# Optimization experiments

Measured on AMD Instinct MI355X. Metric: run time of the kernel, lower is better.

Reference implementation:

```python
import jax, jax.numpy as jnp
import numpy as np

N = 50000
E = 800000
IN_D, HID_D, EMB_D, K = 128, 128, 64, 16
ALPHA = 1.0
NEG_SLOPE = 0.2


def _l2norm(x, eps=1e-12):
    n = jnp.sqrt(jnp.sum(x * x, axis=1, keepdims=True))
    return x / jnp.maximum(n, eps)


def _gat(x, src, dst, W, a_src, a_dst, b, n_nodes):
    # PyG GATConv, heads=1: h = xW; e_ij = leakyrelu(a_src.h_j + a_dst.h_i)
    h = x @ W                                   # [N, D]
    al_s = h @ a_src                            # [N]
    al_d = h @ a_dst                            # [N]
    logits = jax.nn.leaky_relu(al_s[src] + al_d[dst], NEG_SLOPE)  # [E']
    m = jax.ops.segment_max(logits, dst, num_segments=n_nodes)
    ex = jnp.exp(logits - m[dst])
    denom = jax.ops.segment_sum(ex, dst, num_segments=n_nodes)
    alpha = ex / denom[dst]                     # softmax over incoming edges
    out = jax.ops.segment_sum(h[src] * alpha[:, None], dst, num_segments=n_nodes)
    return out + b


def _cluster_prob(z, cluster):
    z2 = jnp.sum(z * z, axis=1, keepdims=True)          # [N,1]
    c2 = jnp.sum(cluster * cluster, axis=1)[None, :]    # [1,K]
    dist = z2 + c2 - 2.0 * (z @ cluster.T)              # [N,K]
    q = 1.0 / (1.0 + dist / ALPHA)
    q = (q + 1e-07) ** ((ALPHA + 1.0) / 2.0)
    return q / jnp.sum(q, axis=1, keepdims=True)


def setup_inputs() -> dict:
    key = jax.random.key(0)
    ks = jax.random.split(key, 20)
    d = {}
    d['x'] = jax.random.normal(ks[0], (N, IN_D), dtype=jnp.float32)
    d['edge_index'] = jax.random.randint(ks[1], (2, E), 0, N, dtype=jnp.int32)
    dims = [(IN_D, HID_D), (HID_D, EMB_D), (EMB_D, HID_D), (HID_D, IN_D)]
    for i, (di, do) in enumerate(dims):
        s = 1.0 / np.sqrt(di)
        d[f'W{i+1}'] = jax.random.normal(ks[2 + 4 * i], (di, do), dtype=jnp.float32) * s
        d[f'a{i+1}s'] = jax.random.normal(ks[3 + 4 * i], (do,), dtype=jnp.float32) * 0.1
        d[f'a{i+1}d'] = jax.random.normal(ks[4 + 4 * i], (do,), dtype=jnp.float32) * 0.1
        d[f'b{i+1}'] = jnp.zeros((do,), dtype=jnp.float32)
    d['cluster'] = jax.random.normal(ks[18], (K, EMB_D), dtype=jnp.float32) * 0.1
    return d


def reference(x, edge_index, W1, a1s, a1d, b1, W2, a2s, a2d, b2,
              W3, a3s, a3d, b3, W4, a4s, a4d, b4, cluster):
    # add self loops (PyG GATConv default)
    loop = jnp.arange(N, dtype=edge_index.dtype)
    src = jnp.concatenate([edge_index[0], loop])
    dst = jnp.concatenate([edge_index[1], loop])

    xn = _l2norm(x)
    h1 = jax.nn.relu(_gat(xn, src, dst, W1, a1s, a1d, b1, N))
    z = _gat(h1, src, dst, W2, a2s, a2d, b2, N)
    z = _l2norm(z)
    d1 = jax.nn.relu(_gat(z, src, dst, W3, a3s, a3d, b3, N))
    x_hat = _gat(d1, src, dst, W4, a4s, a4d, b4, N)
    q = _cluster_prob(z, cluster)
    return (z, x_hat, q)
```

## Files before the change

kernel.cpp:

```cpp
#include <hip/hip_runtime.h>

#define NN 50000
#define NE 800000
#define NBK 196
#define BCAP 8192
#define GEMM_GRID 391
#define WTOT 49152

typedef unsigned int uint;
typedef unsigned short ushort;
typedef __attribute__((ext_vector_type(8))) short short8v;
typedef __attribute__((ext_vector_type(4))) float float4v;

static __device__ __forceinline__ float waveReduceSum(float v) {
#pragma unroll
  for (int o = 32; o > 0; o >>= 1) v += __shfl_xor(v, o);
  return v;
}
static __device__ __forceinline__ float waveReduceMax(float v) {
#pragma unroll
  for (int o = 32; o > 0; o >>= 1) v = fmaxf(v, __shfl_xor(v, o));
  return v;
}
static __device__ __forceinline__ float bf_lo(uint u) { return __uint_as_float(u << 16); }
static __device__ __forceinline__ float bf_hi(uint u) { return __uint_as_float(u & 0xffff0000u); }
static __device__ __forceinline__ uint f2bf(float f) {
  uint u = __float_as_uint(f);
  return (u + 0x7fffu + ((u >> 16) & 1u)) >> 16;
}
static __device__ __forceinline__ int waveInclScan(int v, int lane) {
#pragma unroll
  for (int o = 1; o < 64; o <<= 1) {
    int u = __shfl_up(v, o);
    if (lane >= o) v += u;
  }
  return v;
}
static __device__ __forceinline__ void split8(const float* f, short8v& hi, short8v& lo) {
#pragma unroll
  for (int j = 0; j < 8; ++j) {
    uint h = f2bf(f[j]);
    hi[j] = (short)h;
    float hf = __uint_as_float(h << 16);
    lo[j] = (short)f2bf(f[j] - hf);
  }
}

__global__ void k_zero(int* bcnt) {
  if (threadIdx.x < NBK) bcnt[threadIdx.x] = 0;
}
__global__ __launch_bounds__(256) void k_bucket(
    const int* __restrict__ esrc, const int* __restrict__ edst,
    uint* __restrict__ ebuf, int* __restrict__ bcnt) {
  __shared__ int hist[NBK];
  __shared__ int gbase[NBK];
  int tid = threadIdx.x;
  for (int i = tid; i < NBK; i += 256) hist[i] = 0;
  __syncthreads();
  const int ET = NE + NN;
  int base = blockIdx.x * 4096;
  int myb[16];
  uint mypk[16];
#pragma unroll
  for (int j = 0; j < 16; ++j) {
    int e = base + j * 256 + tid;
    int s, d;
    if (e < NE) { s = esrc[e]; d = edst[e]; }
    else if (e < ET) { s = e - NE; d = s; }
    else { myb[j] = -1; continue; }
    int b = d >> 8;
    myb[j] = b;
    mypk[j] = (uint)s | ((uint)(d & 255) << 16);
    atomicAdd(&hist[b], 1);
  }
  __syncthreads();
  for (int i = tid; i < NBK; i += 256) {
    int h = hist[i];
    gbase[i] = h > 0 ? atomicAdd(&bcnt[i], h) : 0;
    hist[i] = 0;
  }
  __syncthreads();
#pragma unroll
  for (int j = 0; j < 16; ++j) {
    int b = myb[j];
    if (b < 0) continue;
    int r = atomicAdd(&hist[b], 1);
    int pos = gbase[b] + r;
    if (pos < BCAP) ebuf[(size_t)b * BCAP + pos] = mypk[j];
  }
}
__global__ __launch_bounds__(256) void k_csr(
    const uint* __restrict__ ebuf, const int* __restrict__ bcnt,
    int* __restrict__ indptr, int* __restrict__ srcs) {
  __shared__ int h[256];
  __shared__ int cur[256];
  __shared__ int wsm[4];
  __shared__ int bbs;
  int tid = threadIdx.x, b = blockIdx.x;
  int lane = tid & 63, wv = tid >> 6;
  int v = (tid < NBK) ? bcnt[tid] : 0;
  int inc = waveInclScan(v, lane);
  if (lane == 63) wsm[wv] = inc;
  __syncthreads();
  int woff = 0;
  for (int k = 0; k < wv; ++k) woff += wsm[k];
  if (tid == b) bbs = inc - v + woff;
  h[tid] = 0;
  __syncthreads();
  int bbase = bbs;
  int cnt = bcnt[b];
  const uint* eb = ebuf + (size_t)b * BCAP;
  for (int i = tid; i < cnt; i += 256) atomicAdd(&h[eb[i] >> 16], 1);
  __syncthreads();
  int hv = h[tid];
  int inc2 = waveInclScan(hv, lane);
  if (lane == 63) wsm[wv] = inc2;
  __syncthreads();
  int woff2 = 0;
  for (int k = 0; k < wv; ++k) woff2 += wsm[k];
  int nodeExcl = inc2 - hv + woff2;
  int node = b * 256 + tid;
  if (node < NN) indptr[node] = bbase + nodeExcl;
  if (node == NN - 1) indptr[NN] = bbase + nodeExcl + hv;
  cur[tid] = nodeExcl;
  __syncthreads();
  for (int i = tid; i < cnt; i += 256) {
    uint pk = eb[i];
    int r = atomicAdd(&cur[pk >> 16], 1);
    srcs[bbase + r] = (int)(pk & 0xffffu);
  }
}

__global__ void k_wprep(const float* __restrict__ W1, const float* __restrict__ W2,
                        const float* __restrict__ W3, const float* __restrict__ W4,
                        ushort* __restrict__ hi, ushort* __restrict__ lo) {
  int i = blockIdx.x * 256 + threadIdx.x;
  if (i >= WTOT) return;
  const float* W; int DO, base;
  if (i < 16384)      { W = W1; DO = 128; base = 0; }
  else if (i < 24576) { W = W2; DO = 64;  base = 16384; }
  else if (i < 32768) { W = W3; DO = 128; base = 24576; }
  else                { W = W4; DO = 128; base = 32768; }
  int idx = i - base;
  int k = idx / DO, col = idx % DO;
  float w = W[idx];
  uint h = f2bf(w);
  float hf = __uint_as_float(h << 16);
  uint l2 = f2bf(w - hf);
  int CT = DO >> 4;
  int fo = base + (((k >> 5) * CT + (col >> 4)) * 64 + ((col & 15) | (((k >> 3) & 3) << 4))) * 8 + (k & 7);
  hi[fo] = (ushort)h;
  lo[fo] = (ushort)l2;
}

template <int K, int DO, bool NORM>
__global__ __launch_bounds__(256) void k_gemm_mfma(
    const float* __restrict__ X, const ushort* __restrict__ Whi,
    const ushort* __restrict__ Wlo,
    const float* __restrict__ avs, const float* __restrict__ avd,
    ushort* __restrict__ H, float* __restrict__ als, float* __restrict__ ald, int n) {
  constexpr int KS = K / 32, CT = DO / 16;
  constexpr int W4N = K * DO / 8;
  __shared__ ushort sWhi[K * DO];
  __shared__ ushort sWlo[K * DO];
  __shared__ float sas[DO], sad[DO];
  int tid = threadIdx.x;
  for (int i = tid; i < DO; i += 256) { sas[i] = avs[i]; sad[i] = avd[i]; }
  {
    const uint4* ghi = (const uint4*)Whi;
    const uint4* glo = (const uint4*)Wlo;
    uint4* shi = (uint4*)sWhi;
    uint4* slo = (uint4*)sWlo;
    for (int i = tid; i < W4N; i += 256) { shi[i] = ghi[i]; slo[i] = glo[i]; }
  }
  __syncthreads();
  int lane = tid & 63, wv = tid >> 6;
  int ntiles = (n + 63) >> 6;
  for (int tile = blockIdx.x; tile < ntiles; tile += gridDim.x) {
    int r0 = tile * 64 + wv * 16;
    if (r0 >= n) continue;
    int row = r0 + (lane & 15);
    int sub = lane >> 4;
    const float* xrow = X + (size_t)row * K;
    float xr[KS][8];
#pragma unroll
    for (int s = 0; s < KS; ++s) {
      *(float4*)&xr[s][0] = *(const float4*)(xrow + s * 32 + sub * 8);
      *(float4*)&xr[s][4] = *(const float4*)(xrow + s * 32 + sub * 8 + 4);
    }
    if (NORM) {
      float ss = 0.f;
#pragma unroll
      for (int s = 0; s < KS; ++s)
#pragma unroll
        for (int j = 0; j < 8; ++j) ss += xr[s][j] * xr[s][j];
      ss += __shfl_xor(ss, 16);
      ss += __shfl_xor(ss, 32);
      float sc = 1.0f / fmaxf(sqrtf(ss), 1e-12f);
#pragma unroll
      for (int s = 0; s < KS; ++s)
#pragma unroll
        for (int j = 0; j < 8; ++j) xr[s][j] *= sc;
    }
    float4v acc[CT];
#pragma unroll
    for (int c = 0; c < CT; ++c) acc[c] = (float4v){0.f, 0.f, 0.f, 0.f};
#pragma unroll
    for (int s = 0; s < KS; ++s) {
      short8v ahi, alo;
      split8(xr[s], ahi, alo);
#pragma unroll
      for (int c = 0; c < CT; ++c) {
        short8v bhi = *(const short8v*)&sWhi[(s * CT + c) * 512 + lane * 8];
        short8v blo = *(const short8v*)&sWlo[(s * CT + c) * 512 + lane * 8];
        acc[c] = __builtin_amdgcn_mfma_f32_16x16x32_bf16(ahi, bhi, acc[c], 0, 0, 0);
        acc[c] = __builtin_amdgcn_mfma_f32_16x16x32_bf16(ahi, blo, acc[c], 0, 0, 0);
        acc[c] = __builtin_amdgcn_mfma_f32_16x16x32_bf16(alo, bhi, acc[c], 0, 0, 0);
      }
    }
    int rbase = r0 + (sub << 2);
    float alsp[4] = {0.f, 0.f, 0.f, 0.f};
    float aldp[4] = {0.f, 0.f, 0.f, 0.f};
#pragma unroll
    for (int c = 0; c < CT; ++c) {
      int col = (c << 4) + (lane & 15);
      float as_ = sas[col], ad_ = sad[col];
#pragma unroll
      for (int j = 0; j < 4; ++j) {
        float v = acc[c][j];
        alsp[j] += v * as_;
        aldp[j] += v * ad_;
        uint bv = f2bf(v);
        uint nb = __shfl_xor(bv, 1);
        if (!(lane & 1)) {
          *(uint*)&H[(size_t)(rbase + j) * DO + col] = bv | (nb << 16);
        }
      }
    }
#pragma unroll
    for (int j = 0; j < 4; ++j) {
      float vs = alsp[j], vd = aldp[j];
#pragma unroll
      for (int o = 1; o < 16; o <<= 1) { vs += __shfl_xor(vs, o); vd += __shfl_xor(vd, o); }
      if ((lane & 15) == 0) { als[rbase + j] = vs; ald[rbase + j] = vd; }
    }
  }
}

template <int D, int MODE>
__global__ __launch_bounds__(256) void k_attn_aggr(
    const int* __restrict__ indptr, const int* __restrict__ srcs,
    const float* __restrict__ als, const float* __restrict__ ald,
    const ushort* __restrict__ H, const float* __restrict__ bias,
    float* __restrict__ out, const float* __restrict__ cluster,
    float* __restrict__ qout, int n) {
  constexpr int CAP = 256;
  __shared__ float slg[4][CAP];
  __shared__ int ssrc[4][CAP];
  __shared__ float scl[MODE == 2 ? 1024 : 4];
  __shared__ float sz[4][MODE == 2 ? 64 : 4];
  int w = (blockIdx.x * blockDim.x + threadIdx.x) >> 6;
  int l = threadIdx.x & 63;
  int wv = threadIdx.x >> 6;
  if (MODE == 2) {
    for (int i = threadIdx.x; i < 1024; i += 256) scl[i] = cluster[i];
    __syncthreads();
  }
  if (w >= n) return;
  int s0 = indptr[w], s1 = indptr[w + 1];
  int deg = s1 - s0;
  float ad = ald[w];
  float inv;
  float ax = 0.f, ay = 0.f, az = 0.f, aw = 0.f;
  const uint2* Hr = (const uint2*)H;
  if (deg <= CAP) {
    float mx = -1e30f;
    for (int t = l; t < deg; t += 64) {
      int s = srcs[s0 + t];
      float v = als[s] + ad;
      v = v >= 0.f ? v : 0.2f * v;
      ssrc[wv][t] = s;
      slg[wv][t] = v;
      mx = fmaxf(mx, v);
    }
    mx = waveReduceMax(mx);
    float sum = 0.f;
    for (int t = l; t < deg; t += 64) {
      float e = __expf(slg[wv][t] - mx);
      slg[wv][t] = e;
      sum += e;
    }
    sum = waveReduceSum(sum);
    inv = 1.0f / sum;
    if (D == 128) {
      int g = l >> 5, j = l & 31;
      int i = 0;
      for (; i + 16 <= deg; i += 16) {
        float p[8]; int e[8]; uint2 u[8];
#pragma unroll
        for (int r = 0; r < 8; ++r) { int idx = i + 2 * r + g; p[r] = slg[wv][idx]; e[r] = ssrc[wv][idx]; }
#pragma unroll
        for (int r = 0; r < 8; ++r) u[r] = Hr[(size_t)e[r] * 32 + j];
#pragma unroll
        for (int r = 0; r < 8; ++r) {
          ax += p[r] * bf_lo(u[r].x); ay += p[r] * bf_hi(u[r].x);
          az += p[r] * bf_lo(u[r].y); aw += p[r] * bf_hi(u[r].y);
        }
      }
      for (; i + 8 <= deg; i += 8) {
        float p[4]; int e[4]; uint2 u[4];
#pragma unroll
        for (int r = 0; r < 4; ++r) { int idx = i + 2 * r + g; p[r] = slg[wv][idx]; e[r] = ssrc[wv][idx]; }
#pragma unroll
        for (int r = 0; r < 4; ++r) u[r] = Hr[(size_t)e[r] * 32 + j];
#pragma unroll
        for (int r = 0; r < 4; ++r) {
          ax += p[r] * bf_lo(u[r].x); ay += p[r] * bf_hi(u[r].x);
          az += p[r] * bf_lo(u[r].y); aw += p[r] * bf_hi(u[r].y);
        }
      }
      for (; i < deg; i += 2) {
        int idx = i + g;
        if (idx < deg) {
          float p = slg[wv][idx];
          uint2 u = Hr[(size_t)ssrc[wv][idx] * 32 + j];
          ax += p * bf_lo(u.x); ay += p * bf_hi(u.x);
          az += p * bf_lo(u.y); aw += p * bf_hi(u.y);
        }
      }
    } else {
      int g = l >> 4, j = l & 15;
      int i = 0;
      for (; i + 32 <= deg; i += 32) {
        float p[8]; int e[8]; uint2 u[8];
#pragma unroll
        for (int r = 0; r < 8; ++r) { int idx = i + 4 * r + g; p[r] = slg[wv][idx]; e[r] = ssrc[wv][idx]; }
#pragma unroll
        for (int r = 0; r < 8; ++r) u[r] = Hr[(size_t)e[r] * 16 + j];
#pragma unroll
        for (int r = 0; r < 8; ++r) {
          ax += p[r] * bf_lo(u[r].x); ay += p[r] * bf_hi(u[r].x);
          az += p[r] * bf_lo(u[r].y); aw += p[r] * bf_hi(u[r].y);
        }
      }
      for (; i + 16 <= deg; i += 16) {
        float p[4]; int e[4]; uint2 u[4];
#pragma unroll
        for (int r = 0; r < 4; ++r) { int idx = i + 4 * r + g; p[r] = slg[wv][idx]; e[r] = ssrc[wv][idx]; }
#pragma unroll
        for (int r = 0; r < 4; ++r) u[r] = Hr[(size_t)e[r] * 16 + j];
#pragma unroll
        for (int r = 0; r < 4; ++r) {
          ax += p[r] * bf_lo(u[r].x); ay += p[r] * bf_hi(u[r].x);
          az += p[r] * bf_lo(u[r].y); aw += p[r] * bf_hi(u[r].y);
        }
      }
      for (; i < deg; i += 4) {
        int idx = i + g;
        if (idx < deg) {
          float p = slg[wv][idx];
          uint2 u = Hr[(size_t)ssrc[wv][idx] * 16 + j];
          ax += p * bf_lo(u.x); ay += p * bf_hi(u.x);
          az += p * bf_lo(u.y); aw += p * bf_hi(u.y);
        }
      }
    }
  } else {
    float mx = -1e30f;
    for (int t = l; t < deg; t += 64) {
      int s = srcs[s0 + t];
      float v = als[s] + ad;
      v = v >= 0.f ? v : 0.2f * v;
      mx = fmaxf(mx, v);
    }
    mx = waveReduceMax(mx);
    float sum = 0.f;
    for (int t = l; t < deg; t += 64) {
      int s = srcs[s0 + t];
      float v = als[s] + ad;
      v = v >= 0.f ? v : 0.2f * v;
      sum += __expf(v - mx);
    }
    sum = waveReduceSum(sum);
    inv = 1.0f / sum;
    for (int base = 0; base < deg; base += 64) {
      int t = base + l;
      if (t < deg) {
        int s = srcs[s0 + t];
        float v = als[s] + ad;
        v = v >= 0.f ? v : 0.2f * v;
        ssrc[wv][l] = s;
        slg[wv][l] = __expf(v - mx);
      }
      __builtin_amdgcn_wave_barrier();
      int m = min(64, deg - base);
      if (D == 128) {
        int g = l >> 5, j = l & 31;
        for (int i2 = g; i2 < m; i2 += 2) {
          float p = slg[wv][i2];
          uint2 u = Hr[(size_t)ssrc[wv][i2] * 32 + j];
          ax += p * bf_lo(u.x); ay += p * bf_hi(u.x);
          az += p * bf_lo(u.y); aw += p * bf_hi(u.y);
        }
      } else {
        int g = l >> 4, j = l & 15;
        for (int i2 = g; i2 < m; i2 += 4) {
          float p = slg[wv][i2];
          uint2 u = Hr[(size_t)ssrc[wv][i2] * 16 + j];
          ax += p * bf_lo(u.x); ay += p * bf_hi(u.x);
          az += p * bf_lo(u.y); aw += p * bf_hi(u.y);
        }
      }
      __builtin_amdgcn_wave_barrier();
    }
  }
  if (D == 128) {
    ax += __shfl_xor(ax, 32); ay += __shfl_xor(ay, 32);
    az += __shfl_xor(az, 32); aw += __shfl_xor(aw, 32);
    if (l < 32) {
      float4 bv = ((const float4*)bias)[l];
      float v0 = ax * inv + bv.x, v1 = ay * inv + bv.y;
      float v2 = az * inv + bv.z, v3 = aw * inv + bv.w;
      if (MODE == 1) {
        v0 = fmaxf(v0, 0.f); v1 = fmaxf(v1, 0.f);
        v2 = fmaxf(v2, 0.f); v3 = fmaxf(v3, 0.f);
      }
      ((float4*)(out + (size_t)w * 128))[l] = make_float4(v0, v1, v2, v3);
    }
  } else {
    ax += __shfl_xor(ax, 16); ay += __shfl_xor(ay, 16);
    az += __shfl_xor(az, 16); aw += __shfl_xor(aw, 16);
    ax += __shfl_xor(ax, 32); ay += __shfl_xor(ay, 32);
    az += __shfl_xor(az, 32); aw += __shfl_xor(aw, 32);
    int j = l & 15;
    float4 bv = ((const float4*)bias)[j];
    float v0 = ax * inv + bv.x, v1 = ay * inv + bv.y;
    float v2 = az * inv + bv.z, v3 = aw * inv + bv.w;
    if (MODE == 2) {
      float ss = v0 * v0 + v1 * v1 + v2 * v2 + v3 * v3;
      ss += __shfl_xor(ss, 1); ss += __shfl_xor(ss, 2);
      ss += __shfl_xor(ss, 4); ss += __shfl_xor(ss, 8);
      float sc = 1.0f / fmaxf(sqrtf(ss), 1e-12f);
      v0 *= sc; v1 *= sc; v2 *= sc; v3 *= sc;
    }
    if (l < 16) ((float4*)(out + (size_t)w * 64))[j] = make_float4(v0, v1, v2, v3);
    if (MODE == 2) {
      if (l < 16) ((float4*)&sz[wv][0])[j] = make_float4(v0, v1, v2, v3);
      __builtin_amdgcn_wave_barrier();
      int kk = l >> 2, p = l & 3;
      const float* zr = &sz[wv][p * 16];
      const float* cr = &scl[kk * 64 + p * 16];
      float s = 0.f;
#pragma unroll
      for (int d = 0; d < 16; ++d) {
        float df = zr[d] - cr[d];
        s += df * df;
      }
      s += __shfl_xor(s, 1);
      s += __shfl_xor(s, 2);
      float qv = 1.0f / (1.0f + s) + 1e-7f;
      float t = qv;
      t += __shfl_xor(t, 4);
      t += __shfl_xor(t, 8);
      t += __shfl_xor(t, 16);
      t += __shfl_xor(t, 32);
      if (p == 0) qout[(size_t)w * 16 + kk] = qv / t;
    }
  }
}

extern "C" void kernel_launch(void* const* d_in, const int* in_sizes, int n_in,
                              void* d_out, int out_size, void* d_ws, size_t ws_size,
                              hipStream_t stream) {
  const float* x = (const float*)d_in[0];
  const int* ei = (const int*)d_in[1];
  const float* W1 = (const float*)d_in[2];
  const float* a1s = (const float*)d_in[3];
  const float* a1d = (const float*)d_in[4];
  const float* b1 = (const float*)d_in[5];
  const float* W2 = (const float*)d_in[6];
  const float* a2s = (const float*)d_in[7];
  const float* a2d = (const float*)d_in[8];
  const float* b2 = (const float*)d_in[9];
  const float* W3 = (const float*)d_in[10];
  const float* a3s = (const float*)d_in[11];
  const float* a3d = (const float*)d_in[12];
  const float* b3 = (const float*)d_in[13];
  const float* W4 = (const float*)d_in[14];
  const float* a4s = (const float*)d_in[15];
  const float* a4d = (const float*)d_in[16];
  const float* b4 = (const float*)d_in[17];
  const float* cluster = (const float*)d_in[18];

  float* out = (float*)d_out;
  float* z = out;
  float* xhat = out + (size_t)NN * 64;
  float* qout = xhat + (size_t)NN * 128;

  const int ET = NE + NN;
  float* wsf = (float*)d_ws;
  float* X = wsf;          wsf += (size_t)NN * 128;
  ushort* H = (ushort*)wsf; wsf += (size_t)NN * 64;
  float* als = wsf;        wsf += NN;
  float* ald = wsf;        wsf += NN;
  int* indptr = (int*)wsf; wsf += NN + 1;
  int* srcs = (int*)wsf;   wsf += ET;
  uint* ebuf = (uint*)wsf; wsf += (size_t)NBK * BCAP;
  int* bcnt = (int*)wsf;   wsf += NBK;
  ushort* wfhi = (ushort*)wsf; wsf += WTOT / 2;
  ushort* wflo = (ushort*)wsf; wsf += WTOT / 2;

  const int* esrc = ei;
  const int* edst = ei + NE;

  const int TB = 256;
  const int gW = (NN + 3) / 4;
  const int gB = (ET + 4095) / 4096;

  k_zero<<<1, 256, 0, stream>>>(bcnt);
  k_wprep<<<(WTOT + 255) / 256, 256, 0, stream>>>(W1, W2, W3, W4, wfhi, wflo);
  k_bucket<<<gB, 256, 0, stream>>>(esrc, edst, ebuf, bcnt);
  k_csr<<<NBK, 256, 0, stream>>>(ebuf, bcnt, indptr, srcs);

  k_gemm_mfma<128, 128, true><<<GEMM_GRID, 256, 0, stream>>>(
      x, wfhi, wflo, a1s, a1d, H, als, ald, NN);
  k_attn_aggr<128, 1><<<gW, TB, 0, stream>>>(indptr, srcs, als, ald, H, b1, X,
                                             nullptr, nullptr, NN);

  k_gemm_mfma<128, 64, false><<<GEMM_GRID, 256, 0, stream>>>(
      X, wfhi + 16384, wflo + 16384, a2s, a2d, H, als, ald, NN);
  k_attn_aggr<64, 2><<<gW, TB, 0, stream>>>(indptr, srcs, als, ald, H, b2, z,
                                            cluster, qout, NN);

  k_gemm_mfma<64, 128, false><<<GEMM_GRID, 256, 0, stream>>>(
      z, wfhi + 24576, wflo + 24576, a3s, a3d, H, als, ald, NN);
  k_attn_aggr<128, 1><<<gW, TB, 0, stream>>>(indptr, srcs, als, ald, H, b3, X,
                                             nullptr, nullptr, NN);

  k_gemm_mfma<128, 128, false><<<GEMM_GRID, 256, 0, stream>>>(
      X, wfhi + 32768, wflo + 32768, a4s, a4d, H, als, ald, NN);
  k_attn_aggr<128, 0><<<gW, TB, 0, stream>>>(indptr, srcs, als, ald, H, b4, xhat,
                                             nullptr, nullptr, NN);
}
```

Measured before the change: 254.1 us.

## Store hidden features as fp16, fold bucket zeroing into wprep, pad cluster LDS

Intermediate feature matrix H is now stored as fp16 instead of bf16, and the gather-aggregate loops decode it with half-to-float conversions. This trades range for three extra mantissa bits at the same bandwidth. The bucket counter zeroing kernel is merged into the weight-prep kernel to save a launch. The cluster centroid shared array is padded to 68 columns to reduce LDS bank conflicts in the soft-assignment step.

```diff
diff --git a/kernel.cpp b/kernel.cpp
--- a/kernel.cpp
+++ b/kernel.cpp
@@ -1,4 +1,5 @@
 #include <hip/hip_runtime.h>
+#include <hip/hip_fp16.h>
 
 #define NN 50000
 #define NE 800000
@@ -22,11 +23,17 @@
   for (int o = 32; o > 0; o >>= 1) v = fmaxf(v, __shfl_xor(v, o));
   return v;
 }
-static __device__ __forceinline__ float bf_lo(uint u) { return __uint_as_float(u << 16); }
-static __device__ __forceinline__ float bf_hi(uint u) { return __uint_as_float(u & 0xffff0000u); }
 static __device__ __forceinline__ uint f2bf(float f) {
   uint u = __float_as_uint(f);
   return (u + 0x7fffu + ((u >> 16) & 1u)) >> 16;
+}
+static __device__ __forceinline__ float h_lo(uint u) {
+  __half2 h = *(const __half2*)&u;
+  return __half2float(h.x);
+}
+static __device__ __forceinline__ float h_hi(uint u) {
+  __half2 h = *(const __half2*)&u;
+  return __half2float(h.y);
 }
 static __device__ __forceinline__ int waveInclScan(int v, int lane) {
 #pragma unroll
@@ -46,9 +53,6 @@
   }
 }
 
-__global__ void k_zero(int* bcnt) {
-  if (threadIdx.x < NBK) bcnt[threadIdx.x] = 0;
-}
 __global__ __launch_bounds__(256) void k_bucket(
     const int* __restrict__ esrc, const int* __restrict__ edst,
     uint* __restrict__ ebuf, int* __restrict__ bcnt) {
@@ -133,8 +137,10 @@
 
 __global__ void k_wprep(const float* __restrict__ W1, const float* __restrict__ W2,
                         const float* __restrict__ W3, const float* __restrict__ W4,
-                        ushort* __restrict__ hi, ushort* __restrict__ lo) {
+                        ushort* __restrict__ hi, ushort* __restrict__ lo,
+                        int* __restrict__ bcnt) {
   int i = blockIdx.x * 256 + threadIdx.x;
+  if (i < NBK) bcnt[i] = 0;
   if (i >= WTOT) return;
   const float* W; int DO, base;
   if (i < 16384)      { W = W1; DO = 128; base = 0; }
@@ -230,7 +236,7 @@
         float v = acc[c][j];
         alsp[j] += v * as_;
         aldp[j] += v * ad_;
-        uint bv = f2bf(v);
+        uint bv = (uint)__half_as_ushort(__float2half(v));
         uint nb = __shfl_xor(bv, 1);
         if (!(lane & 1)) {
           *(uint*)&H[(size_t)(rbase + j) * DO + col] = bv | (nb << 16);
@@ -257,13 +263,13 @@
   constexpr int CAP = 256;
   __shared__ float slg[4][CAP];
   __shared__ int ssrc[4][CAP];
-  __shared__ float scl[MODE == 2 ? 1024 : 4];
+  __shared__ float scl[MODE == 2 ? 16 : 1][MODE == 2 ? 68 : 1];
   __shared__ float sz[4][MODE == 2 ? 64 : 4];
   int w = (blockIdx.x * blockDim.x + threadIdx.x) >> 6;
   int l = threadIdx.x & 63;
   int wv = threadIdx.x >> 6;
   if (MODE == 2) {
-    for (int i = threadIdx.x; i < 1024; i += 256) scl[i] = cluster[i];
+    for (int i = threadIdx.x; i < 1024; i += 256) scl[i >> 6][i & 63] = cluster[i];
     __syncthreads();
   }
   if (w >= n) return;
@@ -303,8 +309,8 @@
         for (int r = 0; r < 8; ++r) u[r] = Hr[(size_t)e[r] * 32 + j];
 #pragma unroll
         for (int r = 0; r < 8; ++r) {
-          ax += p[r] * bf_lo(u[r].x); ay += p[r] * bf_hi(u[r].x);
-          az += p[r] * bf_lo(u[r].y); aw += p[r] * bf_hi(u[r].y);
+          ax += p[r] * h_lo(u[r].x); ay += p[r] * h_hi(u[r].x);
+          az += p[r] * h_lo(u[r].y); aw += p[r] * h_hi(u[r].y);
         }
       }
       for (; i + 8 <= deg; i += 8) {
@@ -315,8 +321,8 @@
         for (int r = 0; r < 4; ++r) u[r] = Hr[(size_t)e[r] * 32 + j];
 #pragma unroll
         for (int r = 0; r < 4; ++r) {
-          ax += p[r] * bf_lo(u[r].x); ay += p[r] * bf_hi(u[r].x);
-          az += p[r] * bf_lo(u[r].y); aw += p[r] * bf_hi(u[r].y);
+          ax += p[r] * h_lo(u[r].x); ay += p[r] * h_hi(u[r].x);
+          az += p[r] * h_lo(u[r].y); aw += p[r] * h_hi(u[r].y);
         }
       }
       for (; i < deg; i += 2) {
@@ -324,8 +330,8 @@
         if (idx < deg) {
           float p = slg[wv][idx];
           uint2 u = Hr[(size_t)ssrc[wv][idx] * 32 + j];
-          ax += p * bf_lo(u.x); ay += p * bf_hi(u.x);
-          az += p * bf_lo(u.y); aw += p * bf_hi(u.y);
+          ax += p * h_lo(u.x); ay += p * h_hi(u.x);
+          az += p * h_lo(u.y); aw += p * h_hi(u.y);
         }
       }
     } else {
@@ -339,8 +345,8 @@
         for (int r = 0; r < 8; ++r) u[r] = Hr[(size_t)e[r] * 16 + j];
 #pragma unroll
         for (int r = 0; r < 8; ++r) {
-          ax += p[r] * bf_lo(u[r].x); ay += p[r] * bf_hi(u[r].x);
-          az += p[r] * bf_lo(u[r].y); aw += p[r] * bf_hi(u[r].y);
+          ax += p[r] * h_lo(u[r].x); ay += p[r] * h_hi(u[r].x);
+          az += p[r] * h_lo(u[r].y); aw += p[r] * h_hi(u[r].y);
         }
       }
       for (; i + 16 <= deg; i += 16) {
@@ -351,8 +357,8 @@
         for (int r = 0; r < 4; ++r) u[r] = Hr[(size_t)e[r] * 16 + j];
 #pragma unroll
         for (int r = 0; r < 4; ++r) {
-          ax += p[r] * bf_lo(u[r].x); ay += p[r] * bf_hi(u[r].x);
-          az += p[r] * bf_lo(u[r].y); aw += p[r] * bf_hi(u[r].y);
+          ax += p[r] * h_lo(u[r].x); ay += p[r] * h_hi(u[r].x);
+          az += p[r] * h_lo(u[r].y); aw += p[r] * h_hi(u[r].y);
         }
       }
       for (; i < deg; i += 4) {
@@ -360,8 +366,8 @@
         if (idx < deg) {
           float p = slg[wv][idx];
           uint2 u = Hr[(size_t)ssrc[wv][idx] * 16 + j];
-          ax += p * bf_lo(u.x); ay += p * bf_hi(u.x);
-          az += p * bf_lo(u.y); aw += p * bf_hi(u.y);
+          ax += p * h_lo(u.x); ay += p * h_hi(u.x);
+          az += p * h_lo(u.y); aw += p * h_hi(u.y);
         }
       }
     }
@@ -399,16 +405,16 @@
         for (int i2 = g; i2 < m; i2 += 2) {
           float p = slg[wv][i2];
           uint2 u = Hr[(size_t)ssrc[wv][i2] * 32 + j];
-          ax += p * bf_lo(u.x); ay += p * bf_hi(u.x);
-          az += p * bf_lo(u.y); aw += p * bf_hi(u.y);
+          ax += p * h_lo(u.x); ay += p * h_hi(u.x);
+          az += p * h_lo(u.y); aw += p * h_hi(u.y);
         }
       } else {
         int g = l >> 4, j = l & 15;
         for (int i2 = g; i2 < m; i2 += 4) {
           float p = slg[wv][i2];
           uint2 u = Hr[(size_t)ssrc[wv][i2] * 16 + j];
-          ax += p * bf_lo(u.x); ay += p * bf_hi(u.x);
-          az += p * bf_lo(u.y); aw += p * bf_hi(u.y);
+          ax += p * h_lo(u.x); ay += p * h_hi(u.x);
+          az += p * h_lo(u.y); aw += p * h_hi(u.y);
         }
       }
       __builtin_amdgcn_wave_barrier();
@@ -449,7 +455,7 @@
       __builtin_amdgcn_wave_barrier();
       int kk = l >> 2, p = l & 3;
       const float* zr = &sz[wv][p * 16];
-      const float* cr = &scl[kk * 64 + p * 16];
+      const float* cr = &scl[kk][p * 16];
       float s = 0.f;
 #pragma unroll
       for (int d = 0; d < 16; ++d) {
@@ -517,8 +523,7 @@
   const int gW = (NN + 3) / 4;
   const int gB = (ET + 4095) / 4096;
 
-  k_zero<<<1, 256, 0, stream>>>(bcnt);
-  k_wprep<<<(WTOT + 255) / 256, 256, 0, stream>>>(W1, W2, W3, W4, wfhi, wflo);
+  k_wprep<<<(WTOT + 255) / 256, 256, 0, stream>>>(W1, W2, W3, W4, wfhi, wflo, bcnt);
   k_bucket<<<gB, 256, 0, stream>>>(esrc, edst, ebuf, bcnt);
   k_csr<<<NBK, 256, 0, stream>>>(ebuf, bcnt, indptr, srcs);
 
```

Result: faster. 244.9 us (-3.6%).
